# Kernel tuning notes

Hardware: AMD Instinct MI355X
Metric: run time of the kernel (lower is better)

Reference implementation:

```python
import jax, jax.numpy as jnp
import numpy as np
from jax import lax

E = 16          # num_experts
CAP = 256       # capacity
MAX_IT = 3      # max_iterations
LPF = 2.0       # load_penalty_factor
DTEMP = 2.0     # diversity_temp
MIN_USAGE = 0.05
NC = 10         # num_classes
TC = 256        # trunk_channels
B = 2048
MIN_TOK = max(1, int(B * MIN_USAGE))        # 102
K_STATIC = min(B, max(CAP, MIN_TOK))        # static top-k width per expert claim


def setup_inputs() -> dict:
    key = jax.random.key(0)
    ks = jax.random.split(key, 16)
    d = {}
    d['x'] = jax.random.normal(ks[0], (B, 3, 32, 32), jnp.float32)
    chans = [(3, 32), (32, 64), (64, 128), (128, 256)]
    for i, (ci, co) in enumerate(chans, 1):
        d[f'cw{i}'] = jax.random.normal(ks[i], (co, ci, 3, 3), jnp.float32) * (1.0 / np.sqrt(ci * 9))
        d[f'cb{i}'] = jnp.zeros((co,), jnp.float32)
        d[f'g{i}'] = jnp.ones((co,), jnp.float32)
        d[f'be{i}'] = jnp.zeros((co,), jnp.float32)
        d[f'm{i}'] = jnp.zeros((co,), jnp.float32)
        d[f'v{i}'] = jnp.ones((co,), jnp.float32)
    d['gw1'] = jax.random.normal(ks[5], (E, TC, TC // 2), jnp.float32) * 0.05
    d['gb1'] = jnp.zeros((E, TC // 2), jnp.float32)
    d['gw2'] = jax.random.normal(ks[6], (E, TC // 2), jnp.float32) * 0.05
    d['gb2'] = jnp.zeros((E,), jnp.float32)
    d['cls_w'] = jax.random.normal(ks[7], (E, NC, TC), jnp.float32) * 0.01
    d['cls_b'] = jnp.zeros((E, NC), jnp.float32)
    d['usage_ema'] = jnp.ones((E,), jnp.float32) / E
    return d


def _conv_bn_relu(x, w, b, g, beta, m, v):
    y = lax.conv_general_dilated(x, w, (1, 1), 'SAME', dimension_numbers=('NCHW', 'OIHW', 'NCHW'))
    y = y + b[None, :, None, None]
    scale = (g / jnp.sqrt(v + 1e-5))[None, :, None, None]
    return jax.nn.relu((y - m[None, :, None, None]) * scale + beta[None, :, None, None])


def _maxpool2(x):
    return lax.reduce_window(x, -jnp.inf, lax.max, (1, 1, 2, 2), (1, 1, 2, 2), 'VALID')


def _forward(x, cw1, cb1, g1, be1, m1, v1, cw2, cb2, g2, be2, m2, v2,
             cw3, cb3, g3, be3, m3, v3, cw4, cb4, g4, be4, m4, v4,
             gw1, gb1, gw2, gb2, cls_w, cls_b, usage_ema):
    # trunk (eval-mode BN)
    h = _conv_bn_relu(x, cw1, cb1, g1, be1, m1, v1)
    h = _conv_bn_relu(h, cw2, cb2, g2, be2, m2, v2)
    h = _maxpool2(h)
    h = _conv_bn_relu(h, cw3, cb3, g3, be3, m3, v3)
    h = _conv_bn_relu(h, cw4, cb4, g4, be4, m4, v4)
    h = _maxpool2(h)
    feats = h.mean(axis=(2, 3))  # AdaptiveAvgPool2d(1)+Flatten -> [B, TC]

    # per-expert classifier heads
    logits_e = jnp.einsum('bd,ecd->bec', feats, cls_w) + cls_b[None]  # [B,E,NC]
    probs = jax.nn.softmax(logits_e, axis=2)
    ent = -(probs * jnp.log(jnp.clip(probs, 1e-12))).sum(axis=2)      # [B,E]
    confidence = -ent

    # per-expert gates (vectorized over experts); dropout is identity in eval
    hidden = jax.nn.relu(jnp.einsum('bd,edh->beh', feats, gw1) + gb1[None])
    expert_scores = (jnp.einsum('beh,eh->be', hidden, gw2) + gb2[None]) / DTEMP

    routing_scores = 0.6 * expert_scores + 0.4 * confidence - LPF * usage_ema[None]

    # iterative capacity-constrained routing (eval: expert order 0..E-1)
    D = jnp.zeros((B, E), bool)
    loads = jnp.zeros((E,), jnp.float32)
    avail = jnp.ones((B,), bool)
    ranks = jnp.arange(K_STATIC)
    for it in range(MAX_IT):
        # penalty from loads at the START of the iteration
        pscores = routing_scores - (it + 1) * LPF * loads[None]
        for j in range(E):
            sj = jnp.where(avail, pscores[:, j], -jnp.inf)
            vc = avail.sum().astype(jnp.int32)
            rc = jnp.maximum(0, CAP - loads[j].astype(jnp.int32))
            ntc = jnp.where((rc == 0) | (vc == 0), 0,
                            jnp.maximum(jnp.minimum(rc, vc), jnp.minimum(MIN_TOK, vc)))
            _, idx = lax.top_k(sj, K_STATIC)
            take = ranks < ntc
            claimed = jnp.zeros((B,), bool).at[idx].set(take)
            D = D.at[:, j].set(D[:, j] | claimed)
            avail = avail & ~claimed
            loads = loads.at[j].add(ntc.astype(jnp.float32))

    # fallback: sequentially assign leftover tokens to least-loaded of top-3
    def fb(carry, inp):
        Dc, lc = carry
        sc, av, i = inp
        _, t3 = lax.top_k(sc, 3)
        best = t3[jnp.argmin(lc[t3])]
        Dc = Dc.at[i, best].set(Dc[i, best] | av)
        lc = lc.at[best].add(av.astype(jnp.float32))
        return (Dc, lc), None

    (D, loads), _ = lax.scan(fb, (D, loads), (routing_scores, avail, jnp.arange(B)))

    Df = D.astype(jnp.float32)
    active = routing_scores * Df
    active = active - active.max(axis=1, keepdims=True)
    weights = jax.nn.softmax(active + (Df - 1.0) * 1e9, axis=1)
    final_logits = (weights[:, :, None] * logits_e).sum(axis=1)
    return final_logits, routing_scores, D


def reference(x, cw1, cb1, g1, be1, m1, v1, cw2, cb2, g2, be2, m2, v2,
              cw3, cb3, g3, be3, m3, v3, cw4, cb4, g4, be4, m4, v4,
              gw1, gb1, gw2, gb2, cls_w, cls_b, usage_ema):
    return _forward(x, cw1, cb1, g1, be1, m1, v1, cw2, cb2, g2, be2, m2, v2,
                    cw3, cb3, g3, be3, m3, v3, cw4, cb4, g4, be4, m4, v4,
                    gw1, gb1, gw2, gb2, cls_w, cls_b, usage_ema)
```

## Files before the change

kernel.cpp:

```cpp
#include <hip/hip_runtime.h>

typedef __attribute__((ext_vector_type(8))) short short8;
typedef __attribute__((ext_vector_type(4))) float f32x4;

__device__ __forceinline__ unsigned short f2bf(float f) {
  unsigned u = __float_as_uint(f);
  unsigned r = (u + 0x7fffu + ((u >> 16) & 1u)) >> 16;
  return (unsigned short)r;
}
__device__ __forceinline__ float bf2f(unsigned short h) {
  return __uint_as_float(((unsigned)h) << 16);
}

__global__ __launch_bounds__(256) void bnprep_kernel(
    const float* __restrict__ g, const float* __restrict__ be,
    const float* __restrict__ m, const float* __restrict__ v,
    const float* __restrict__ b, float* __restrict__ A, float* __restrict__ C, int n)
{
  int i = blockIdx.x * 256 + threadIdx.x;
  if (i < n) {
    float s = g[i] / sqrtf(v[i] + 1e-5f);
    A[i] = s;
    C[i] = (b[i] - m[i]) * s + be[i];
  }
}

__global__ __launch_bounds__(256) void wprep2_kernel(
    const float* __restrict__ w, unsigned short* __restrict__ wPk, int CO, int CI)
{
  int NCB = CI / 32, NF = CO / 16;
  int total = 9 * NCB * NF * 64;
  int idx = blockIdx.x * 256 + threadIdx.x;
  if (idx >= total) return;
  int lane = idx & 63;
  int unit = idx >> 6;
  int f = unit % NF;
  int cb = (unit / NF) % NCB;
  int s = unit / (NF * NCB);
  int co = f * 16 + (lane & 15);
  int ci0 = cb * 32 + (lane >> 4) * 8;
  long base = (long)unit * 1024 + lane * 8;
  #pragma unroll
  for (int j = 0; j < 8; ++j) {
    float v = w[((long)co * CI + ci0 + j) * 9 + s];
    unsigned short h = f2bf(v);
    unsigned short l = f2bf(v - bf2f(h));
    wPk[base + j] = h;
    wPk[base + 512 + j] = l;
  }
}

__global__ __launch_bounds__(256) void conv1_kernel(
    const float* __restrict__ in, const float* __restrict__ wgt,
    const float* __restrict__ Ap, const float* __restrict__ Cp,
    unsigned short* __restrict__ out)
{
  __shared__ alignas(16) float smem[3 * 432 + 864];
  const int tid = threadIdx.x;
  const int img = blockIdx.x;
  const int by = (blockIdx.y >> 1) * 16, bx = (blockIdx.y & 1) * 16;
  const int r0 = (tid & 63) >> 4, xx = tid & 15, cog = tid >> 6;

  float acc[4][8];
  #pragma unroll
  for (int i = 0; i < 4; ++i)
    #pragma unroll
    for (int j = 0; j < 8; ++j) acc[i][j] = 0.f;

  for (int e = tid; e < 972; e += 256) {
    int ci = e / 324, rem = e - ci * 324;
    int rr = rem / 18, cc = rem - rr * 18;
    int gy = by + rr - 1, gx = bx + cc - 1;
    float v = 0.f;
    if (gy >= 0 && gy < 32 && gx >= 0 && gx < 32)
      v = in[(long)img * 3072 + ci * 1024 + gy * 32 + gx];
    smem[ci * 432 + rr * 24 + cc] = v;
  }
  for (int e = tid; e < 864; e += 256) {
    int co = e & 31, rem = e >> 5;
    smem[1296 + rem * 32 + co] = wgt[(long)co * 27 + rem];
  }
  __syncthreads();
  for (int ci = 0; ci < 3; ++ci) {
    #pragma unroll
    for (int k = 0; k < 9; ++k) {
      int ky = k / 3, kx = k - 3 * (k / 3);
      const float4* w4 = (const float4*)(smem + 1296 + (ci * 9 + k) * 32 + cog * 8);
      float4 w0 = w4[0], w1 = w4[1];
      #pragma unroll
      for (int i = 0; i < 4; ++i) {
        float iv = smem[ci * 432 + (r0 + 4 * i + ky) * 24 + xx + kx];
        acc[i][0] += iv * w0.x; acc[i][1] += iv * w0.y;
        acc[i][2] += iv * w0.z; acc[i][3] += iv * w0.w;
        acc[i][4] += iv * w1.x; acc[i][5] += iv * w1.y;
        acc[i][6] += iv * w1.z; acc[i][7] += iv * w1.w;
      }
    }
  }
  #pragma unroll
  for (int j = 0; j < 8; ++j) {
    int co = cog * 8 + j;
    float Ar = Ap[co], Cr = Cp[co];
    #pragma unroll
    for (int i = 0; i < 4; ++i) {
      float vv = fmaxf(acc[i][j] * Ar + Cr, 0.f);
      unsigned short h = f2bf(vv);
      unsigned short l = f2bf(vv - bf2f(h));
      long px = (long)img * 1024 + (by + r0 + 4 * i) * 32 + bx + xx;
      out[px * 64 + co] = h;
      out[px * 64 + 32 + co] = l;
    }
  }
}

template<int H, int CI, int CO, int COB, int TY, int TX, int MODE>
__global__ __launch_bounds__(512, 2) void convmf4_kernel(
    const unsigned short* __restrict__ actIn, const unsigned short* __restrict__ wPk,
    const float* __restrict__ Ap, const float* __restrict__ Cp,
    void* __restrict__ outP)
{
  constexpr int NCB = CI / 32;
  constexpr int NF  = CO / 16;
  constexpr int NCOG = COB / 64;
  constexpr int NPXG = 8 / NCOG;
  constexpr int ROWS_PG = TY / NPXG;
  constexpr int FRX = TX / 16;
  constexpr int PXW = TX + 2;
  constexpr int PXT = (TY + 2) * PXW;
  constexpr int PLSTR = PXT * 8 + 8;
  constexpr int TILES_Y = H / TY;
  constexpr int CBLK = CO / COB;
  constexpr int TPI = TILES_Y * CBLK;
  constexpr int PIX_IN = 2 * CI;
  __shared__ alignas(16) unsigned short smem[8 * PLSTR];

  const int nwg = gridDim.x;
  const int orig = blockIdx.x;
  const int q = nwg >> 3, r = nwg & 7;
  const int xcd = orig & 7, pos = orig >> 3;
  const int bx = (xcd < r ? xcd * (q + 1) : r * (q + 1) + (xcd - r) * q) + pos;

  const int img = bx / TPI;
  const int sub = bx % TPI;
  const int tY0 = (sub % TILES_Y) * TY;
  const int blkco = sub / TILES_Y;

  const int tid = threadIdx.x;
  const int lane = tid & 63;
  const int lx = lane & 15, kg = lane >> 4;
  const int w = tid >> 6;
  const int pxg = w % NPXG, cog = w / NPXG;

  f32x4 acc[4][4];
  #pragma unroll
  for (int i = 0; i < 4; ++i)
    #pragma unroll
    for (int j = 0; j < 4; ++j) acc[i][j] = (f32x4){0.f, 0.f, 0.f, 0.f};

  for (int cb = 0; cb < NCB; ++cb) {
    if (cb) __syncthreads();
    for (int t2 = tid; t2 < PXT * 8; t2 += 512) {
      int px = t2 >> 3, c = t2 & 7;
      int ry = px / PXW, rx = px - ry * PXW;
      int gy = tY0 + ry - 1, gx = rx - 1;
      float4 v = (float4){0.f, 0.f, 0.f, 0.f};
      if (gy >= 0 && gy < H && gx >= 0 && gx < H) {
        int coff = (c < 4) ? (cb * 32 + c * 8) : (CI + cb * 32 + (c - 4) * 8);
        v = *(const float4*)(actIn + ((long)img * H * H + gy * H + gx) * PIX_IN + coff);
      }
      *(float4*)(smem + c * PLSTR + px * 8) = v;
    }
    __syncthreads();

    for (int s = 0; s < 9; ++s) {
      const int ky = s / 3, kx = s - 3 * (s / 3);
      const long ub = ((long)(s * NCB + cb) * NF + blkco * (COB / 16) + cog * 4) * 1024
                      + lane * 8;
      short8 bh[4], bl[4];
      #pragma unroll
      for (int nf = 0; nf < 4; ++nf) {
        bh[nf] = *(const short8*)(wPk + ub + nf * 1024);
        bl[nf] = *(const short8*)(wPk + ub + nf * 1024 + 512);
      }
      #pragma unroll
      for (int mf = 0; mf < 4; ++mf) {
        const int yoff = (FRX == 2) ? (mf >> 1) : mf;
        const int xb = (FRX == 2) ? ((mf & 1) * 16) : 0;
        const int y = pxg * ROWS_PG + yoff;
        const int pxa = (y + ky) * PXW + xb + kx + lx;
        short8 ah = *(const short8*)(smem + kg * PLSTR + pxa * 8);
        short8 al = *(const short8*)(smem + (kg + 4) * PLSTR + pxa * 8);
        #pragma unroll
        for (int nf = 0; nf < 4; ++nf)
          acc[mf][nf] = __builtin_amdgcn_mfma_f32_16x16x32_bf16(ah, bh[nf], acc[mf][nf], 0, 0, 0);
        #pragma unroll
        for (int nf = 0; nf < 4; ++nf)
          acc[mf][nf] = __builtin_amdgcn_mfma_f32_16x16x32_bf16(ah, bl[nf], acc[mf][nf], 0, 0, 0);
        #pragma unroll
        for (int nf = 0; nf < 4; ++nf)
          acc[mf][nf] = __builtin_amdgcn_mfma_f32_16x16x32_bf16(al, bh[nf], acc[mf][nf], 0, 0, 0);
      }
    }
  }
  __syncthreads();

  float Ar[4], Cr[4];
  #pragma unroll
  for (int nf = 0; nf < 4; ++nf) {
    int co = blkco * COB + cog * 64 + nf * 16 + lx;
    Ar[nf] = Ap[co]; Cr[nf] = Cp[co];
  }

  if (MODE == 0) {
    unsigned short* outA = (unsigned short*)outP;
    unsigned short* slice = smem + w * 2048;
    #pragma unroll
    for (int mf = 0; mf < 4; ++mf) {
      int y = tY0 + pxg * ROWS_PG + mf;
      #pragma unroll
      for (int rr = 0; rr < 4; ++rr) {
        int x = 4 * kg + rr;
        #pragma unroll
        for (int nf = 0; nf < 4; ++nf) {
          float vv = fmaxf(acc[mf][nf][rr] * Ar[nf] + Cr[nf], 0.f);
          unsigned short h = f2bf(vv);
          unsigned short l = f2bf(vv - bf2f(h));
          slice[(x * 2 + 0) * 64 + nf * 16 + lx] = h;
          slice[(x * 2 + 1) * 64 + nf * 16 + lx] = l;
        }
      }
      #pragma unroll
      for (int v = 0; v < 4; ++v) {
        int hoff = lane * 8 + v * 512;
        int x2 = hoff >> 7, rem = hoff & 127;
        int seg = rem >> 6, inner = rem & 63;
        short8 d = *(const short8*)(slice + hoff);
        *(short8*)(outA + ((long)img * 256 + y * 16 + x2) * (2 * CO)
                   + seg * CO + blkco * COB + cog * 64 + inner) = d;
      }
    }
  } else if (MODE == 1) {
    unsigned short* outA = (unsigned short*)outP;
    unsigned short* slice = smem + w * 2048;
    const int py = (tY0 >> 1) + pxg;
    #pragma unroll
    for (int xf = 0; xf < 2; ++xf) {
      #pragma unroll
      for (int rp = 0; rp < 2; ++rp) {
        int ox = xf * 8 + 2 * kg + rp;
        #pragma unroll
        for (int nf = 0; nf < 4; ++nf) {
          float v0 = fmaxf(fmaxf(acc[xf][nf][2 * rp], acc[xf][nf][2 * rp + 1]),
                           fmaxf(acc[xf + 2][nf][2 * rp], acc[xf + 2][nf][2 * rp + 1]));
          float vv = fmaxf(v0 * Ar[nf] + Cr[nf], 0.f);
          unsigned short h = f2bf(vv);
          unsigned short l = f2bf(vv - bf2f(h));
          slice[(ox * 2 + 0) * 64 + nf * 16 + lx] = h;
          slice[(ox * 2 + 1) * 64 + nf * 16 + lx] = l;
        }
      }
    }
    #pragma unroll
    for (int v = 0; v < 4; ++v) {
      int hoff = lane * 8 + v * 512;
      int x2 = hoff >> 7, rem = hoff & 127;
      int seg = rem >> 6, inner = rem & 63;
      short8 d = *(const short8*)(slice + hoff);
      *(short8*)(outA + ((long)img * 256 + py * 16 + x2) * (2 * CO)
                 + seg * CO + inner) = d;
    }
  } else {
    float psum[4] = {0.f, 0.f, 0.f, 0.f};
    #pragma unroll
    for (int nf = 0; nf < 4; ++nf) {
      #pragma unroll
      for (int mfp = 0; mfp < 2; ++mfp) {
        #pragma unroll
        for (int rp = 0; rp < 2; ++rp) {
          float v = fmaxf(fmaxf(acc[2 * mfp][nf][2 * rp], acc[2 * mfp][nf][2 * rp + 1]),
                          fmaxf(acc[2 * mfp + 1][nf][2 * rp], acc[2 * mfp + 1][nf][2 * rp + 1]));
          psum[nf] += fmaxf(v * Ar[nf] + Cr[nf], 0.f);
        }
      }
    }
    #pragma unroll
    for (int nf = 0; nf < 4; ++nf) {
      psum[nf] += __shfl_xor(psum[nf], 16);
      psum[nf] += __shfl_xor(psum[nf], 32);
    }
    __syncthreads();
    float* sR = (float*)smem;
    if (kg == 0) {
      #pragma unroll
      for (int nf = 0; nf < 4; ++nf) sR[w * 64 + nf * 16 + lx] = psum[nf];
    }
    __syncthreads();
    if (tid < COB) {
      int ct = tid >> 6, ci_ = tid & 63;
      float s = 0.f;
      #pragma unroll
      for (int p = 0; p < NPXG; ++p) s += sR[(ct * NPXG + p) * 64 + ci_];
      ((float*)outP)[(long)img * 256 + blkco * COB + tid] = s * (1.f / 64.f);
    }
  }
}

__global__ __launch_bounds__(256) void heads2_kernel(
    const float* __restrict__ feats, const float* __restrict__ gw1,
    const float* __restrict__ gb1, const float* __restrict__ gw2,
    const float* __restrict__ gb2, const float* __restrict__ clsw,
    const float* __restrict__ clsb, const float* __restrict__ usage,
    float* __restrict__ logits_e, float* __restrict__ rs_out)
{
  __shared__ float sF[64 * 257];
  __shared__ float sLg[4 * 64 * 10];
  __shared__ float sRed[4 * 64];
  const int tid = threadIdx.x;
  const int b0 = blockIdx.x * 64;
  const int e  = blockIdx.y;

  for (int idx = tid; idx < 64 * 64; idx += 256) {
    int t = idx >> 6, dg = idx & 63;
    float4 v = ((const float4*)(feats + (long)(b0 + t) * 256))[dg];
    float* p = sF + t * 257 + dg * 4;
    p[0] = v.x; p[1] = v.y; p[2] = v.z; p[3] = v.w;
  }
  __syncthreads();

  const int t  = tid & 63;
  const int hw = __builtin_amdgcn_readfirstlane(tid >> 6);

  {
    float acc[10];
    #pragma unroll
    for (int c = 0; c < 10; ++c) acc[c] = 0.f;
    const float* fp = sF + t * 257 + hw * 64;
    const float* cw = clsw + (long)e * 2560 + hw * 64;
    for (int dd = 0; dd < 64; ++dd) {
      float f = fp[dd];
      #pragma unroll
      for (int c = 0; c < 10; ++c) acc[c] += f * cw[c * 256 + dd];
    }
    #pragma unroll
    for (int c = 0; c < 10; ++c) sLg[(hw * 64 + t) * 10 + c] = acc[c];
  }
  {
    float gacc[32];
    #pragma unroll
    for (int j = 0; j < 32; ++j) gacc[j] = 0.f;
    const float* wb = gw1 + ((long)e * 256) * 128 + hw * 32;
    const float* fp = sF + t * 257;
    for (int d = 0; d < 256; ++d) {
      float f = fp[d];
      const float4* w4 = (const float4*)(wb + (long)d * 128);
      #pragma unroll
      for (int qq = 0; qq < 8; ++qq) {
        float4 wv = w4[qq];
        gacc[4 * qq + 0] += f * wv.x; gacc[4 * qq + 1] += f * wv.y;
        gacc[4 * qq + 2] += f * wv.z; gacc[4 * qq + 3] += f * wv.w;
      }
    }
    float s = 0.f;
    const float* b1 = gb1 + e * 128 + hw * 32;
    const float* w2 = gw2 + e * 128 + hw * 32;
    #pragma unroll
    for (int j = 0; j < 32; ++j) s += fmaxf(gacc[j] + b1[j], 0.f) * w2[j];
    sRed[hw * 64 + t] = s;
  }
  __syncthreads();

  if (tid < 64) {
    float es = (sRed[t] + sRed[64 + t] + sRed[128 + t] + sRed[192 + t] + gb2[e]) * 0.5f;
    float lg[10];
    #pragma unroll
    for (int c = 0; c < 10; ++c)
      lg[c] = sLg[t * 10 + c] + sLg[(64 + t) * 10 + c]
            + sLg[(128 + t) * 10 + c] + sLg[(192 + t) * 10 + c] + clsb[e * 10 + c];
    float mx = lg[0];
    #pragma unroll
    for (int c = 1; c < 10; ++c) mx = fmaxf(mx, lg[c]);
    float S = 0.f, ps[10];
    #pragma unroll
    for (int c = 0; c < 10; ++c) { ps[c] = expf(lg[c] - mx); S += ps[c]; }
    float inv = 1.f / S, ent = 0.f;
    #pragma unroll
    for (int c = 0; c < 10; ++c) { float p = ps[c] * inv; ent -= p * logf(fmaxf(p, 1e-12f)); }
    float rsv = 0.6f * es + 0.4f * (-ent) - 2.0f * usage[e];
    rs_out[(long)(b0 + t) * 16 + e] = rsv;
    #pragma unroll
    for (int c = 0; c < 10; ++c)
      logits_e[((long)(b0 + t) * 16 + e) * 10 + c] = lg[c];
  }
}

__global__ __launch_bounds__(1024) void sort_kernel(
    const float* __restrict__ rs, unsigned* __restrict__ sortedIdx)
{
  __shared__ unsigned long long sk[2048];
  const int e = blockIdx.x;
  const unsigned tid = threadIdx.x;
  for (int i = tid; i < 2048; i += 1024) {
    float f = rs[(long)i * 16 + e];
    unsigned u = __float_as_uint(f);
    u ^= (u >> 31) ? 0xFFFFFFFFu : 0x80000000u;
    sk[i] = ((unsigned long long)(~u) << 32) | (unsigned)i;
  }
  for (unsigned k = 2; k <= 2048; k <<= 1) {
    for (unsigned j = k >> 1; j > 0; j >>= 1) {
      __syncthreads();
      unsigned i = ((tid & ~(j - 1)) << 1) | (tid & (j - 1));
      unsigned p = i | j;
      bool asc = ((i & k) == 0);
      unsigned long long a = sk[i], b = sk[p];
      if ((a > b) == asc) { sk[i] = b; sk[p] = a; }
    }
  }
  __syncthreads();
  for (int i = tid; i < 2048; i += 1024)
    sortedIdx[(long)e * 2048 + i] = (unsigned)(sk[i] & 0xFFFFFFFFull);
}

__global__ __launch_bounds__(1024) void routing_kernel(
    const unsigned* __restrict__ sortedIdx, const float* __restrict__ rs,
    float* __restrict__ Dout, unsigned* __restrict__ dmaskOut)
{
  __shared__ unsigned char sAvail[2048];
  __shared__ unsigned sDm[2048];
  __shared__ int sLoads[16];
  __shared__ int sWaveCnt[16];
  __shared__ int sNtc, sVC;
  const int tid = threadIdx.x;
  const int lane = tid & 63, wave = tid >> 6;
  for (int i = tid; i < 2048; i += 1024) { sAvail[i] = 1; sDm[i] = 0; }
  if (tid < 16) sLoads[tid] = 0;
  if (tid == 0) sVC = 2048;
  __syncthreads();
  for (int it = 0; it < 3; ++it) {
    for (int j = 0; j < 16; ++j) {
      if (tid == 0) {
        int rc = 256 - sLoads[j]; if (rc < 0) rc = 0;
        int vc = sVC, ntc = 0;
        if (rc > 0 && vc > 0) {
          int a = rc < vc ? rc : vc;
          int b2 = vc < 102 ? vc : 102;
          ntc = a > b2 ? a : b2;
        }
        sNtc = ntc; sLoads[j] += ntc; sVC -= ntc;
      }
      __syncthreads();
      const int ntc = sNtc;
      if (ntc > 0) {
        int base = 0;
        for (int p = 0; p < 2; ++p) {
          int i = p * 1024 + tid;
          unsigned tok = sortedIdx[(long)j * 2048 + i];
          int fl = sAvail[tok] ? 1 : 0;
          unsigned long long bm = __ballot(fl);
          if (lane == 0) sWaveCnt[wave] = __popcll(bm);
          __syncthreads();
          int off = base;
          for (int w = 0; w < wave; ++w) off += sWaveCnt[w];
          int pre = off + __popcll(bm & ((1ull << lane) - 1ull));
          if (fl && pre < ntc) { sAvail[tok] = 0; sDm[tok] |= (1u << j); }
          int tot = base;
          for (int w = 0; w < 16; ++w) tot += sWaveCnt[w];
          base = tot;
          __syncthreads();
        }
      }
      __syncthreads();
    }
  }
  if (tid == 0 && sVC > 0) {
    for (int i = 0; i < 2048; ++i) {
      if (!sAvail[i]) continue;
      float s0 = -3.4e38f, s1 = s0, s2 = s0; int e0 = 0, e1 = 0, e2 = 0;
      for (int e = 0; e < 16; ++e) {
        float s = rs[i * 16 + e];
        if (s > s0)      { s2 = s1; e2 = e1; s1 = s0; e1 = e0; s0 = s; e0 = e; }
        else if (s > s1) { s2 = s1; e2 = e1; s1 = s;  e1 = e; }
        else if (s > s2) { s2 = s;  e2 = e; }
      }
      int best = e0, bl = sLoads[e0];
      if (sLoads[e1] < bl) { best = e1; bl = sLoads[e1]; }
      if (sLoads[e2] < bl) { best = e2; bl = sLoads[e2]; }
      sDm[i] |= (1u << best);
      sLoads[best] += 1;
    }
  }
  __syncthreads();
  for (int idx = tid; idx < 2048 * 16; idx += 1024) {
    int tok = idx >> 4, e = idx & 15;
    Dout[idx] = ((sDm[tok] >> e) & 1u) ? 1.0f : 0.0f;
  }
  for (int i = tid; i < 2048; i += 1024) dmaskOut[i] = sDm[i];
}

__global__ __launch_bounds__(256) void combine_kernel(
    const unsigned* __restrict__ dmask, const float* __restrict__ rs,
    const float* __restrict__ L, float* __restrict__ out)
{
  int i = blockIdx.x * 256 + threadIdx.x;
  if (i >= 2048) return;
  unsigned dm = dmask[i];
  float r[16];
  #pragma unroll
  for (int e = 0; e < 16; ++e) r[e] = rs[i * 16 + e];
  float mx = -3.4e38f;
  #pragma unroll
  for (int e = 0; e < 16; ++e) {
    float v = ((dm >> e) & 1u) ? r[e] : 0.0f;
    mx = fmaxf(mx, v);
  }
  float w[16], S = 0.f;
  #pragma unroll
  for (int e = 0; e < 16; ++e) {
    w[e] = ((dm >> e) & 1u) ? expf(r[e] - mx) : 0.0f;
    S += w[e];
  }
  float inv = 1.f / S;
  #pragma unroll
  for (int c = 0; c < 10; ++c) {
    float a = 0.f;
    #pragma unroll
    for (int e = 0; e < 16; ++e) a += w[e] * L[((long)i * 16 + e) * 10 + c];
    out[i * 10 + c] = a * inv;
  }
}

extern "C" void kernel_launch(void* const* d_in, const int* in_sizes, int n_in,
                              void* d_out, int out_size, void* d_ws, size_t ws_size,
                              hipStream_t stream)
{
  const float* x    = (const float*)d_in[0];
  const float* cw1  = (const float*)d_in[1];
  const float* cb1  = (const float*)d_in[2];
  const float* g1   = (const float*)d_in[3];
  const float* be1  = (const float*)d_in[4];
  const float* m1   = (const float*)d_in[5];
  const float* v1   = (const float*)d_in[6];
  const float* cw2  = (const float*)d_in[7];
  const float* cb2  = (const float*)d_in[8];
  const float* g2   = (const float*)d_in[9];
  const float* be2  = (const float*)d_in[10];
  const float* m2   = (const float*)d_in[11];
  const float* v2   = (const float*)d_in[12];
  const float* cw3  = (const float*)d_in[13];
  const float* cb3  = (const float*)d_in[14];
  const float* g3   = (const float*)d_in[15];
  const float* be3  = (const float*)d_in[16];
  const float* m3   = (const float*)d_in[17];
  const float* v3   = (const float*)d_in[18];
  const float* cw4  = (const float*)d_in[19];
  const float* cb4  = (const float*)d_in[20];
  const float* g4   = (const float*)d_in[21];
  const float* be4  = (const float*)d_in[22];
  const float* m4   = (const float*)d_in[23];
  const float* v4   = (const float*)d_in[24];
  const float* gw1  = (const float*)d_in[25];
  const float* gb1  = (const float*)d_in[26];
  const float* gw2  = (const float*)d_in[27];
  const float* gb2  = (const float*)d_in[28];
  const float* clsw = (const float*)d_in[29];
  const float* clsb = (const float*)d_in[30];
  const float* usage = (const float*)d_in[31];

  float* out = (float*)d_out;
  float* ws  = (float*)d_ws;

  float* A1 = ws + 0;   float* C1 = ws + 32;
  float* A2 = ws + 64;  float* C2 = ws + 128;
  float* A3 = ws + 192; float* C3 = ws + 320;
  float* A4 = ws + 448; float* C4 = ws + 704;
  float* feats   = ws + 1024;
  float* logitsE = ws + 525312;
  unsigned* sortedIdx = (unsigned*)(ws + 852992);
  unsigned* dmask     = (unsigned*)(ws + 885760);
  unsigned short* wPk2 = (unsigned short*)(ws + 887808);
  unsigned short* wPk3 = (unsigned short*)(ws + 906240);
  unsigned short* wPk4 = (unsigned short*)(ws + 979968);
  const long bufBase = 1274880;

  long wsFloats = (long)(ws_size / 4);
  long availF = wsFloats - bufBase;
  long chunkL = availF / 49152;
  int chunk = (int)(chunkL < 1 ? 1 : (chunkL > 2048 ? 2048 : chunkL));

  bnprep_kernel<<<1, 256, 0, stream>>>(g1, be1, m1, v1, cb1, A1, C1, 32);
  bnprep_kernel<<<1, 256, 0, stream>>>(g2, be2, m2, v2, cb2, A2, C2, 64);
  bnprep_kernel<<<1, 256, 0, stream>>>(g3, be3, m3, v3, cb3, A3, C3, 128);
  bnprep_kernel<<<1, 256, 0, stream>>>(g4, be4, m4, v4, cb4, A4, C4, 256);
  wprep2_kernel<<<(2304 + 255) / 256, 256, 0, stream>>>(cw2, wPk2, 64, 32);
  wprep2_kernel<<<(9216 + 255) / 256, 256, 0, stream>>>(cw3, wPk3, 128, 64);
  wprep2_kernel<<<(36864 + 255) / 256, 256, 0, stream>>>(cw4, wPk4, 256, 128);

  unsigned short* bufA = (unsigned short*)(ws + bufBase);
  unsigned short* bufB = bufA + (long)chunk * 65536;

  for (int ib = 0; ib < 2048; ib += chunk) {
    int n = 2048 - ib; if (n > chunk) n = chunk;
    conv1_kernel<<<dim3(n, 4), 256, 0, stream>>>(x + (long)ib * 3072, cw1, A1, C1, bufA);
    convmf4_kernel<32, 32, 64, 64, 16, 32, 1>
        <<<dim3(n * 2), 512, 0, stream>>>(bufA, wPk2, A2, C2, bufB);
    convmf4_kernel<16, 64, 128, 128, 16, 16, 0>
        <<<dim3(n), 512, 0, stream>>>(bufB, wPk3, A3, C3, bufA);
    convmf4_kernel<16, 128, 256, 128, 16, 16, 2>
        <<<dim3(n * 2), 512, 0, stream>>>(bufA, wPk4, A4, C4, feats + (long)ib * 256);
  }

  float* rsOut = out + 20480;
  heads2_kernel<<<dim3(32, 16), 256, 0, stream>>>(feats, gw1, gb1, gw2, gb2,
                                                  clsw, clsb, usage, logitsE, rsOut);
  sort_kernel<<<16, 1024, 0, stream>>>(rsOut, sortedIdx);
  routing_kernel<<<1, 1024, 0, stream>>>(sortedIdx, rsOut, out + 53248, dmask);
  combine_kernel<<<8, 256, 0, stream>>>(dmask, rsOut, logitsE, out);
}
```

Before: 1.413 ms.

## Fuse conv1 into conv2 kernel, computing conv1 halo tile in shared memory

Replaces the separate conv1 kernel and the MODE 1 conv2 kernel with one fused kernel. Each block computes conv1 with BN, ReLU and the bf16 hi/lo split for its tile plus a halo directly into LDS, then runs the conv2 MFMA loop and the pooled epilogue. This removes the global write and re-read of the 32x32x64 conv1 activation and one launch per chunk. In exchange, halo pixels are recomputed redundantly and the fp32 conv1 stage holds 32 accumulators per thread, which raises register pressure under launch bounds 512,2.

```diff
diff --git a/kernel.cpp b/kernel.cpp
--- a/kernel.cpp
+++ b/kernel.cpp
@@ -50,66 +50,165 @@
   }
 }
 
-__global__ __launch_bounds__(256) void conv1_kernel(
-    const float* __restrict__ in, const float* __restrict__ wgt,
-    const float* __restrict__ Ap, const float* __restrict__ Cp,
-    unsigned short* __restrict__ out)
-{
-  __shared__ alignas(16) float smem[3 * 432 + 864];
+__global__ __launch_bounds__(512, 2) void conv12_kernel(
+    const float* __restrict__ xin, const float* __restrict__ cw1,
+    const float* __restrict__ A1p, const float* __restrict__ C1p,
+    const unsigned short* __restrict__ wPk, const float* __restrict__ Ap,
+    const float* __restrict__ Cp, unsigned short* __restrict__ outA)
+{
+  constexpr int TY = 16, TX = 32;
+  constexpr int PXW = TX + 2;
+  constexpr int PXT = (TY + 2) * PXW;
+  constexpr int PLSTR = PXT * 8 + 8;
+  constexpr int CO = 64, NF = 4;
+  __shared__ alignas(16) unsigned short smem[8 * PLSTR];
+  __shared__ alignas(16) float sx[2160];
+  __shared__ alignas(16) float sw[864];
+
+  const int nwg = gridDim.x;
+  const int orig = blockIdx.x;
+  const int q = nwg >> 3, r = nwg & 7;
+  const int xcd = orig & 7, pos = orig >> 3;
+  const int bx = (xcd < r ? xcd * (q + 1) : r * (q + 1) + (xcd - r) * q) + pos;
+
+  const int img = bx >> 1;
+  const int tY0 = (bx & 1) * 16;
+
   const int tid = threadIdx.x;
-  const int img = blockIdx.x;
-  const int by = (blockIdx.y >> 1) * 16, bx = (blockIdx.y & 1) * 16;
-  const int r0 = (tid & 63) >> 4, xx = tid & 15, cog = tid >> 6;
-
-  float acc[4][8];
+  const int lane = tid & 63;
+  const int lx = lane & 15, kg = lane >> 4;
+  const int w = tid >> 6;
+
+  for (int i = tid; i < 2160; i += 512) {
+    int c = i / 720, rem = i - c * 720;
+    int yy = rem / 36, xx2 = rem - yy * 36;
+    int gy = tY0 + yy - 2, gx = xx2 - 2;
+    sx[i] = (gy >= 0 && gy < 32 && gx >= 0 && gx < 32)
+            ? xin[(long)img * 3072 + c * 1024 + gy * 32 + gx] : 0.f;
+  }
+  for (int i = tid; i < 864; i += 512) {
+    int co = i & 31, kk = i >> 5;
+    sw[kk * 32 + co] = cw1[(long)co * 27 + kk];
+  }
+  __syncthreads();
+
+  for (int p = 0; p < 2; ++p) {
+    int px = p * 512 + tid;
+    if (px < PXT) {
+      int ry = px / PXW, rx = px - ry * PXW;
+      int gy = tY0 + ry - 1, gx = rx - 1;
+      if (gy >= 0 && gy < 32 && gx >= 0 && gx < 32) {
+        float acc[32];
+        #pragma unroll
+        for (int j = 0; j < 32; ++j) acc[j] = 0.f;
+        #pragma unroll
+        for (int c = 0; c < 3; ++c) {
+          #pragma unroll
+          for (int k = 0; k < 9; ++k) {
+            int dy = k / 3, dx = k - 3 * (k / 3);
+            float iv = sx[c * 720 + (ry + dy) * 36 + rx + dx];
+            const float4* w4 = (const float4*)(sw + (c * 9 + k) * 32);
+            #pragma unroll
+            for (int q2 = 0; q2 < 8; ++q2) {
+              float4 wv = w4[q2];
+              acc[4 * q2 + 0] += iv * wv.x; acc[4 * q2 + 1] += iv * wv.y;
+              acc[4 * q2 + 2] += iv * wv.z; acc[4 * q2 + 3] += iv * wv.w;
+            }
+          }
+        }
+        #pragma unroll
+        for (int cc = 0; cc < 4; ++cc) {
+          short8 hv, lv;
+          #pragma unroll
+          for (int j = 0; j < 8; ++j) {
+            int co = cc * 8 + j;
+            float vv = fmaxf(acc[co] * A1p[co] + C1p[co], 0.f);
+            unsigned short h = f2bf(vv);
+            hv[j] = (short)h;
+            lv[j] = (short)f2bf(vv - bf2f(h));
+          }
+          *(short8*)(smem + cc * PLSTR + px * 8) = hv;
+          *(short8*)(smem + (cc + 4) * PLSTR + px * 8) = lv;
+        }
+      } else {
+        short8 zz = {0, 0, 0, 0, 0, 0, 0, 0};
+        #pragma unroll
+        for (int cc = 0; cc < 8; ++cc)
+          *(short8*)(smem + cc * PLSTR + px * 8) = zz;
+      }
+    }
+  }
+  __syncthreads();
+
+  f32x4 acc[4][4];
   #pragma unroll
   for (int i = 0; i < 4; ++i)
     #pragma unroll
-    for (int j = 0; j < 8; ++j) acc[i][j] = 0.f;
-
-  for (int e = tid; e < 972; e += 256) {
-    int ci = e / 324, rem = e - ci * 324;
-    int rr = rem / 18, cc = rem - rr * 18;
-    int gy = by + rr - 1, gx = bx + cc - 1;
-    float v = 0.f;
-    if (gy >= 0 && gy < 32 && gx >= 0 && gx < 32)
-      v = in[(long)img * 3072 + ci * 1024 + gy * 32 + gx];
-    smem[ci * 432 + rr * 24 + cc] = v;
-  }
-  for (int e = tid; e < 864; e += 256) {
-    int co = e & 31, rem = e >> 5;
-    smem[1296 + rem * 32 + co] = wgt[(long)co * 27 + rem];
-  }
-  __syncthreads();
-  for (int ci = 0; ci < 3; ++ci) {
-    #pragma unroll
-    for (int k = 0; k < 9; ++k) {
-      int ky = k / 3, kx = k - 3 * (k / 3);
-      const float4* w4 = (const float4*)(smem + 1296 + (ci * 9 + k) * 32 + cog * 8);
-      float4 w0 = w4[0], w1 = w4[1];
-      #pragma unroll
-      for (int i = 0; i < 4; ++i) {
-        float iv = smem[ci * 432 + (r0 + 4 * i + ky) * 24 + xx + kx];
-        acc[i][0] += iv * w0.x; acc[i][1] += iv * w0.y;
-        acc[i][2] += iv * w0.z; acc[i][3] += iv * w0.w;
-        acc[i][4] += iv * w1.x; acc[i][5] += iv * w1.y;
-        acc[i][6] += iv * w1.z; acc[i][7] += iv * w1.w;
-      }
-    }
-  }
-  #pragma unroll
-  for (int j = 0; j < 8; ++j) {
-    int co = cog * 8 + j;
-    float Ar = Ap[co], Cr = Cp[co];
-    #pragma unroll
-    for (int i = 0; i < 4; ++i) {
-      float vv = fmaxf(acc[i][j] * Ar + Cr, 0.f);
-      unsigned short h = f2bf(vv);
-      unsigned short l = f2bf(vv - bf2f(h));
-      long px = (long)img * 1024 + (by + r0 + 4 * i) * 32 + bx + xx;
-      out[px * 64 + co] = h;
-      out[px * 64 + 32 + co] = l;
-    }
+    for (int j = 0; j < 4; ++j) acc[i][j] = (f32x4){0.f, 0.f, 0.f, 0.f};
+
+  for (int s = 0; s < 9; ++s) {
+    const int ky = s / 3, kx = s - 3 * (s / 3);
+    const long ub = ((long)(s * NF)) * 1024 + lane * 8;
+    short8 bh[4], bl[4];
+    #pragma unroll
+    for (int nf = 0; nf < 4; ++nf) {
+      bh[nf] = *(const short8*)(wPk + ub + nf * 1024);
+      bl[nf] = *(const short8*)(wPk + ub + nf * 1024 + 512);
+    }
+    #pragma unroll
+    for (int mf = 0; mf < 4; ++mf) {
+      const int yoff = mf >> 1;
+      const int xb = (mf & 1) * 16;
+      const int y = w * 2 + yoff;
+      const int pxa = (y + ky) * PXW + xb + kx + lx;
+      short8 ah = *(const short8*)(smem + kg * PLSTR + pxa * 8);
+      short8 al = *(const short8*)(smem + (kg + 4) * PLSTR + pxa * 8);
+      #pragma unroll
+      for (int nf = 0; nf < 4; ++nf)
+        acc[mf][nf] = __builtin_amdgcn_mfma_f32_16x16x32_bf16(ah, bh[nf], acc[mf][nf], 0, 0, 0);
+      #pragma unroll
+      for (int nf = 0; nf < 4; ++nf)
+        acc[mf][nf] = __builtin_amdgcn_mfma_f32_16x16x32_bf16(ah, bl[nf], acc[mf][nf], 0, 0, 0);
+      #pragma unroll
+      for (int nf = 0; nf < 4; ++nf)
+        acc[mf][nf] = __builtin_amdgcn_mfma_f32_16x16x32_bf16(al, bh[nf], acc[mf][nf], 0, 0, 0);
+    }
+  }
+  __syncthreads();
+
+  float Ar[4], Cr[4];
+  #pragma unroll
+  for (int nf = 0; nf < 4; ++nf) {
+    int co = nf * 16 + lx;
+    Ar[nf] = Ap[co]; Cr[nf] = Cp[co];
+  }
+
+  unsigned short* slice = smem + w * 2048;
+  const int py = (tY0 >> 1) + w;
+  #pragma unroll
+  for (int xf = 0; xf < 2; ++xf) {
+    #pragma unroll
+    for (int rp = 0; rp < 2; ++rp) {
+      int ox = xf * 8 + 2 * kg + rp;
+      #pragma unroll
+      for (int nf = 0; nf < 4; ++nf) {
+        float v0 = fmaxf(fmaxf(acc[xf][nf][2 * rp], acc[xf][nf][2 * rp + 1]),
+                         fmaxf(acc[xf + 2][nf][2 * rp], acc[xf + 2][nf][2 * rp + 1]));
+        float vv = fmaxf(v0 * Ar[nf] + Cr[nf], 0.f);
+        unsigned short h = f2bf(vv);
+        unsigned short l = f2bf(vv - bf2f(h));
+        slice[(ox * 2 + 0) * 64 + nf * 16 + lx] = h;
+        slice[(ox * 2 + 1) * 64 + nf * 16 + lx] = l;
+      }
+    }
+  }
+  #pragma unroll
+  for (int v = 0; v < 4; ++v) {
+    int hoff = lane * 8 + v * 512;
+    int x2 = hoff >> 7, rem = hoff & 127;
+    int seg = rem >> 6, inner = rem & 63;
+    short8 d = *(const short8*)(slice + hoff);
+    *(short8*)(outA + ((long)img * 256 + py * 16 + x2) * 128 + seg * 64 + inner) = d;
   }
 }
 
@@ -238,36 +337,6 @@
         *(short8*)(outA + ((long)img * 256 + y * 16 + x2) * (2 * CO)
                    + seg * CO + blkco * COB + cog * 64 + inner) = d;
       }
-    }
-  } else if (MODE == 1) {
-    unsigned short* outA = (unsigned short*)outP;
-    unsigned short* slice = smem + w * 2048;
-    const int py = (tY0 >> 1) + pxg;
-    #pragma unroll
-    for (int xf = 0; xf < 2; ++xf) {
-      #pragma unroll
-      for (int rp = 0; rp < 2; ++rp) {
-        int ox = xf * 8 + 2 * kg + rp;
-        #pragma unroll
-        for (int nf = 0; nf < 4; ++nf) {
-          float v0 = fmaxf(fmaxf(acc[xf][nf][2 * rp], acc[xf][nf][2 * rp + 1]),
-                           fmaxf(acc[xf + 2][nf][2 * rp], acc[xf + 2][nf][2 * rp + 1]));
-          float vv = fmaxf(v0 * Ar[nf] + Cr[nf], 0.f);
-          unsigned short h = f2bf(vv);
-          unsigned short l = f2bf(vv - bf2f(h));
-          slice[(ox * 2 + 0) * 64 + nf * 16 + lx] = h;
-          slice[(ox * 2 + 1) * 64 + nf * 16 + lx] = l;
-        }
-      }
-    }
-    #pragma unroll
-    for (int v = 0; v < 4; ++v) {
-      int hoff = lane * 8 + v * 512;
-      int x2 = hoff >> 7, rem = hoff & 127;
-      int seg = rem >> 6, inner = rem & 63;
-      short8 d = *(const short8*)(slice + hoff);
-      *(short8*)(outA + ((long)img * 256 + py * 16 + x2) * (2 * CO)
-                 + seg * CO + inner) = d;
     }
   } else {
     float psum[4] = {0.f, 0.f, 0.f, 0.f};
@@ -599,9 +668,8 @@
 
   for (int ib = 0; ib < 2048; ib += chunk) {
     int n = 2048 - ib; if (n > chunk) n = chunk;
-    conv1_kernel<<<dim3(n, 4), 256, 0, stream>>>(x + (long)ib * 3072, cw1, A1, C1, bufA);
-    convmf4_kernel<32, 32, 64, 64, 16, 32, 1>
-        <<<dim3(n * 2), 512, 0, stream>>>(bufA, wPk2, A2, C2, bufB);
+    conv12_kernel<<<dim3(n * 2), 512, 0, stream>>>(
+        x + (long)ib * 3072, cw1, A1, C1, wPk2, A2, C2, bufB);
     convmf4_kernel<16, 64, 128, 128, 16, 16, 0>
         <<<dim3(n), 512, 0, stream>>>(bufB, wPk3, A3, C3, bufA);
     convmf4_kernel<16, 128, 256, 128, 16, 16, 2>
```

Result: slower. 1.943 ms (+37.5%).
